# Kernel optimization log

Hardware: AMD Instinct MI355X
Metric: run time of the kernel (lower is better)

## Reference

```python
import jax, jax.numpy as jnp
import numpy as np
from jax import lax

NPOINT = 1024
NSAMPLE = 32
RADIUS = 0.2
EPS = 1e-5  # BatchNorm eps (torch default)
MLP = [64, 64, 128]
IN_CHANNEL = 6  # 3 (relative xyz) + 3 (point features)


def setup_inputs() -> dict:
    key = jax.random.key(0)
    ks = jax.random.split(key, 2 + len(MLP))
    B, N, D = 16, 4096, 3
    inp = {
        "xyz": jax.random.uniform(ks[0], (B, N, 3), jnp.float32),
        "points": jax.random.normal(ks[1], (B, N, D), jnp.float32),
    }
    last = IN_CHANNEL
    for i, co in enumerate(MLP):
        inp[f"w{i}"] = jax.random.normal(ks[2 + i], (co, last), jnp.float32) * (1.0 / np.sqrt(last))
        inp[f"b{i}"] = jnp.zeros((co,), jnp.float32)
        inp[f"gamma{i}"] = jnp.ones((co,), jnp.float32)
        inp[f"beta{i}"] = jnp.zeros((co,), jnp.float32)
        last = co
    return inp


def index_points(points, idx):
    # points: [B, N, C]; idx: [B, S] or [B, S, K] -> [B, S, C] or [B, S, K, C]
    B, C = points.shape[0], points.shape[-1]
    flat = idx.reshape(B, -1)
    out = jnp.take_along_axis(points, flat[:, :, None], axis=1)
    return out.reshape(idx.shape + (C,))


def farthest_point_sample(xyz, npoint):
    # Deterministic FPS (start index 0 per batch); torch version uses a random start.
    B, N, _ = xyz.shape

    def step(carry, _):
        dist, far = carry
        centroid = jnp.take_along_axis(xyz, far[:, None, None], axis=1)  # [B,1,3]
        d = jnp.sum((xyz - centroid) ** 2, axis=-1)  # [B,N]
        dist = jnp.minimum(dist, d)
        return (dist, jnp.argmax(dist, axis=-1).astype(jnp.int32)), far

    init = (jnp.full((B, N), 1e10, dtype=xyz.dtype), jnp.zeros((B,), jnp.int32))
    _, fars = lax.scan(step, init, None, length=npoint)  # [npoint, B]
    return jnp.transpose(fars)  # [B, npoint]


def square_distance(src, dst):
    # [B,N,3] x [B,M,3] -> [B,N,M] squared distances
    d = -2.0 * jnp.einsum('bnc,bmc->bnm', src, dst)
    d = d + jnp.sum(src ** 2, -1)[:, :, None]
    d = d + jnp.sum(dst ** 2, -1)[:, None, :]
    return d


def query_ball_point(radius, nsample, xyz, new_xyz):
    B, N, _ = xyz.shape
    sqr = square_distance(new_xyz, xyz)  # [B,S,N]
    idx = jnp.broadcast_to(jnp.arange(N, dtype=jnp.int32), sqr.shape)
    idx = jnp.where(sqr > radius ** 2, N, idx)
    idx = jnp.sort(idx, axis=-1)[:, :, :nsample]  # [B,S,nsample]
    first = idx[:, :, :1]
    return jnp.where(idx == N, first, idx)


def reference(xyz, points,
              w0, b0, gamma0, beta0,
              w1, b1, gamma1, beta1,
              w2, b2, gamma2, beta2):
    fps_idx = farthest_point_sample(xyz, NPOINT)          # [B,S]
    new_xyz = index_points(xyz, fps_idx)                  # [B,S,3]
    idx = query_ball_point(RADIUS, NSAMPLE, xyz, new_xyz)  # [B,S,K]
    grouped_xyz = index_points(xyz, idx) - new_xyz[:, :, None, :]  # [B,S,K,3]
    grouped_pts = index_points(points, idx)               # [B,S,K,D]
    x = jnp.concatenate([grouped_xyz, grouped_pts], axis=-1)  # [B,S,K,3+D]

    for (w, b, g, be) in [(w0, b0, gamma0, beta0),
                          (w1, b1, gamma1, beta1),
                          (w2, b2, gamma2, beta2)]:
        x = jnp.einsum('bskc,oc->bsko', x, w) + b  # 1x1 Conv2d
        mean = x.mean(axis=(0, 1, 2))
        var = x.var(axis=(0, 1, 2))  # biased, matches BN training-mode normalization
        x = jax.nn.relu(g * (x - mean) * lax.rsqrt(var + EPS) + be)

    new_points = x.max(axis=2)  # max-pool over the K neighbor dim -> [B,S,mlp[-1]]
    return new_xyz, new_points
```

## Files before the change

kernel.cpp:

```cpp
#include <hip/hip_runtime.h>
#include <hip/hip_fp16.h>
#include <stdint.h>

#define B_ 16
#define N_ 4096
#define S_ 1024
#define K_ 32
#define NQ_ (B_*S_)
#define NPIX_ (NQ_*K_)
#define OUTNP_ (NQ_*3)
#define EPS_ 1e-5f


#define DPPMAX64(x, CTRL) do { \
  unsigned _lo = (unsigned)(x); unsigned _hi = (unsigned)((x)>>32); \
  unsigned _plo = (unsigned)__builtin_amdgcn_update_dpp((int)_lo,(int)_lo,(CTRL),0xF,0xF,false); \
  unsigned _phi = (unsigned)__builtin_amdgcn_update_dpp((int)_hi,(int)_hi,(CTRL),0xF,0xF,false); \
  unsigned long long _p = (((unsigned long long)_phi)<<32)|_plo; \
  if (_p > (x)) (x) = _p; \
} while(0)

#define DPPMAXF(r, CTRL) do { \
  float _t = __int_as_float(__builtin_amdgcn_update_dpp(__float_as_int(r),__float_as_int(r),(CTRL),0xF,0xF,false)); \
  (r) = fmaxf((r), _t); \
} while(0)

__global__ __launch_bounds__(512) void k_fps(const float* __restrict__ xyz,
                                             float* __restrict__ out,
                                             float* __restrict__ nx) {
  const int b = blockIdx.x;
  const int t = threadIdx.x;
  const int lane = t & 63, wid = t >> 6;
  __shared__ int SX[N_], SY[N_], SZ[N_];
  __shared__ unsigned long long kbuf[2][8];
  const float* xb = xyz + (size_t)b * N_ * 3;
  for (int j = t; j < N_; j += 512) {
    SX[j] = (int)(xb[j*3+0] * 536870912.0f);
    SY[j] = (int)(xb[j*3+1] * 536870912.0f);
    SZ[j] = (int)(xb[j*3+2] * 536870912.0f);
  }
  __syncthreads();
  int PX[8], PY[8], PZ[8];
  unsigned long long key[8];
#pragma unroll
  for (int i = 0; i < 8; ++i) {
    const int j = t*8 + i;
    PX[i] = SX[j]; PY[i] = SY[j]; PZ[i] = SZ[j];
    key[i] = ~0ull;
  }
  int far = 0, farA = 0, farB = 0;
  for (int it = 0; it < S_; ++it) {
    if (it == t)       farA = far;
    if (it == t + 512) farB = far;
    if (it == S_-1) break;
    const int cx = SX[far], cy = SY[far], cz = SZ[far];
    unsigned long long best = 0;
#pragma unroll
    for (int i = 0; i < 8; ++i) {
      const int dx = PX[i]-cx, dy = PY[i]-cy, dz = PZ[i]-cz;
      unsigned long long nk = (unsigned long long)(unsigned)(4095 - (t*8 + i));
      nk += (unsigned long long)((long long)dx*dx);
      nk += (unsigned long long)((long long)dy*dy);
      nk += (unsigned long long)((long long)dz*dz);
      if (nk < key[i]) key[i] = nk;
      if (key[i] > best) best = key[i];
    }
    DPPMAX64(best, 0x111);
    DPPMAX64(best, 0x112);
    DPPMAX64(best, 0x114);
    DPPMAX64(best, 0x118);
    DPPMAX64(best, 0x142);
    DPPMAX64(best, 0x143);
    if (lane == 63) kbuf[it & 1][wid] = best;
    __syncthreads();
    unsigned long long g = kbuf[it & 1][lane & 7];
    DPPMAX64(g, 0x111); DPPMAX64(g, 0x112); DPPMAX64(g, 0x114);
    far = 4095 - (__builtin_amdgcn_readlane((int)(unsigned)g, 7) & 4095);
  }
  {
    const float s = 1.862645149230957e-9f;
    const float ax = (float)SX[farA]*s, ay = (float)SY[farA]*s, az = (float)SZ[farA]*s;
    const float bx = (float)SX[farB]*s, by = (float)SY[farB]*s, bz = (float)SZ[farB]*s;
    const int oA = (b*S_ + t)*3;
    const int oB = (b*S_ + t + 512)*3;
    out[oA] = ax; out[oA+1] = ay; out[oA+2] = az;
    nx[oA]  = ax; nx[oA+1]  = ay; nx[oA+2]  = az;
    out[oB] = bx; out[oB+1] = by; out[oB+2] = bz;
    nx[oB]  = bx; nx[oB+1]  = by; nx[oB+2]  = bz;
  }
}

__global__ __launch_bounds__(256) void k_ball(const float* __restrict__ xyz,
                                              const float* __restrict__ nx,
                                              int* __restrict__ idx,
                                              const float* __restrict__ w0,
                                              const float* __restrict__ w1,
                                              const float* __restrict__ w2,
                                              float* __restrict__ w0t,
                                              float* __restrict__ w1t,
                                              float* __restrict__ w2t) {
  if (blockIdx.x == NQ_/4) {
    const int t = threadIdx.x;
    for (int i = t; i < 64*6; i += 256)  { int o = i/6,  c = i%6;  w0t[c*64  + o] = w0[i]; }
    for (int i = t; i < 64*64; i += 256) { int o = i>>6, c = i&63; w1t[c*64  + o] = w1[i]; }
    for (int i = t; i < 128*64; i += 256){ int o = i>>6, c = i&63; w2t[c*128 + o] = w2[i]; }
    return;
  }
  const int lane = threadIdx.x & 63;
  const int q = blockIdx.x * 4 + (threadIdx.x >> 6);
  const int b = q >> 10;
  const float* xb = xyz + (size_t)b * N_ * 3;
  const double qx = (double)nx[q*3+0], qy = (double)nx[q*3+1], qz = (double)nx[q*3+2];
  const double qq = qx*qx + qy*qy + qz*qz;
  const double r2 = 0.2 * 0.2;
  int found = 0, first_j = 0;
  bool have_first = false;
  for (int c = 0; c < N_/64; ++c) {
    const int j = c*64 + lane;
    const double px = (double)xb[j*3+0], py = (double)xb[j*3+1], pz = (double)xb[j*3+2];
    const double dot = px*qx + py*qy + pz*qz;
    const double pp  = px*px + py*py + pz*pz;
    const double d   = qq + pp - 2.0*dot;
    const bool hit = (d <= r2);
    const unsigned long long mask = __ballot(hit);
    if (!have_first && mask) { first_j = c*64 + (__ffsll(mask) - 1); have_first = true; }
    const int pos = found + (int)__popcll(mask & ((1ull << lane) - 1ull));
    if (hit && pos < K_) idx[q*K_ + pos] = j;
    found += (int)__popcll(mask);
    if (found >= K_) break;
  }
  const int cnt = found < K_ ? found : K_;
  if (lane >= cnt && lane < K_) idx[q*K_ + lane] = first_j;
}

__global__ __launch_bounds__(256) void k_momw(const float* __restrict__ xyz,
                                              const float* __restrict__ points,
                                              const float* __restrict__ nx,
                                              const int* __restrict__ idx,
                                              float* __restrict__ momp) {
  const int tid = blockIdx.x * blockDim.x + threadIdx.x;
  float m[6] = {0,0,0,0,0,0};
  float M2[21];
#pragma unroll
  for (int u = 0; u < 21; ++u) M2[u] = 0.0f;
  int js[8], qs[8];
#pragma unroll
  for (int r = 0; r < 8; ++r) {
    const int pix = tid + (r << 16);
    js[r] = idx[pix]; qs[r] = pix >> 5;
  }
#pragma unroll
  for (int r = 0; r < 8; ++r) {
    const int b = qs[r] >> 10;
    const float* xp = xyz    + (size_t)(b*N_ + js[r])*3;
    const float* pq = points + (size_t)(b*N_ + js[r])*3;
    const float* nq = nx + qs[r]*3;
    float g[6];
    g[0] = xp[0]-nq[0]; g[1] = xp[1]-nq[1]; g[2] = xp[2]-nq[2];
    g[3] = pq[0]; g[4] = pq[1]; g[5] = pq[2];
#pragma unroll
    for (int i = 0; i < 6; ++i) m[i] += g[i];
    int u = 0;
#pragma unroll
    for (int i = 0; i < 6; ++i)
#pragma unroll
      for (int jj = i; jj < 6; ++jj) { M2[u] = fmaf(g[i], g[jj], M2[u]); ++u; }
  }
#pragma unroll
  for (int i = 0; i < 6; ++i)
#pragma unroll
    for (int s = 1; s < 64; s <<= 1) m[i] += __shfl_xor(m[i], s);
#pragma unroll
  for (int u = 0; u < 21; ++u)
#pragma unroll
    for (int s = 1; s < 64; s <<= 1) M2[u] += __shfl_xor(M2[u], s);
  if ((threadIdx.x & 63) == 0) {
    const int w = blockIdx.x * 4 + (threadIdx.x >> 6);
    float* dst = momp + w*32;
#pragma unroll
    for (int i = 0; i < 6; ++i) dst[i] = m[i];
#pragma unroll
    for (int u = 0; u < 21; ++u) dst[6+u] = M2[u];
  }
}

__global__ void k_fin0r(const float* __restrict__ momp,
                        const float* __restrict__ w0, const float* __restrict__ b0,
                        const float* __restrict__ g0, const float* __restrict__ be0,
                        float* __restrict__ pr) {
  __shared__ float part[8][32];
  __shared__ float red[32];
  const int t = threadIdx.x;
  const int c = t & 31, p = t >> 5;
  float a = 0.f;
  for (int w = p; w < 1024; w += 8) a += momp[w*32 + c];
  part[p][c] = a;
  __syncthreads();
  if (t < 32) {
    float s = 0.f;
#pragma unroll
    for (int pp = 0; pp < 8; ++pp) s += part[pp][c];
    red[c] = s;
  }
  __syncthreads();
  if (t < 64) {
    const float inv = 1.0f / (float)NPIX_;
    float m1[6];
#pragma unroll
    for (int i = 0; i < 6; ++i) m1[i] = red[i] * inv;
    float M2[6][6];
    int u = 0;
#pragma unroll
    for (int i = 0; i < 6; ++i)
#pragma unroll
      for (int jj = i; jj < 6; ++jj) { float v = red[6+u]*inv; M2[i][jj] = v; M2[jj][i] = v; ++u; }
    float w[6];
#pragma unroll
    for (int i = 0; i < 6; ++i) w[i] = w0[t*6+i];
    float ml = 0.0f;
#pragma unroll
    for (int i = 0; i < 6; ++i) ml += w[i]*m1[i];
    float e2 = 0.0f;
#pragma unroll
    for (int i = 0; i < 6; ++i)
#pragma unroll
      for (int jj = 0; jj < 6; ++jj) e2 += w[i]*w[jj]*M2[i][jj];
    const float var = e2 - ml*ml;
    const float mean = ml + b0[t];
    const float sc = g0[t] * rsqrtf(var + EPS_);
    pr[t] = sc; pr[64+t] = be0[t] - mean*sc;
  }
}

__global__ void k_fin1r(const float* __restrict__ s1p,
                        const float* __restrict__ g1, const float* __restrict__ be1,
                        float* __restrict__ pr) {
  __shared__ float pa[4][64], pb[4][64];
  const int t = threadIdx.x;
  const int c = t & 63, p = t >> 6;
  const int wq = c >> 4, u = c & 15;
  float sa = 0.f, sb = 0.f;
  for (int blk = p; blk < 1024; blk += 4) {
    const int w = blk*4 + wq;
    sa += s1p[w*32 + u];
    sb += s1p[w*32 + 16 + u];
  }
  pa[p][c] = sa; pb[p][c] = sb;
  __syncthreads();
  if (t < 64) {
    const float A  = pa[0][t]+pa[1][t]+pa[2][t]+pa[3][t];
    const float Bq = pb[0][t]+pb[1][t]+pb[2][t]+pb[3][t];
    const float inv = 1.0f / (float)NPIX_;
    const float mean = A*inv;
    const float var = Bq*inv - mean*mean;
    const float sc = g1[t] * rsqrtf(var + EPS_);
    pr[128+t] = sc; pr[192+t] = be1[t] - mean*sc;
  }
}

__global__ void k_fin2r(const float* __restrict__ s2p,
                        const float* __restrict__ g2, const float* __restrict__ be2,
                        float* __restrict__ pr) {
  __shared__ float pa[2][128], pb[2][128];
  const int t = threadIdx.x;
  const int c = t & 127, p = t >> 7;
  const int wq = c >> 5, u = c & 31;
  float sa = 0.f, sb = 0.f;
  for (int blk = p; blk < 1024; blk += 2) {
    const int w = blk*4 + wq;
    sa += s2p[w*64 + u];
    sb += s2p[w*64 + 32 + u];
  }
  pa[p][c] = sa; pb[p][c] = sb;
  __syncthreads();
  if (t < 128) {
    const float A  = pa[0][t]+pa[1][t];
    const float Bq = pb[0][t]+pb[1][t];
    const float inv = 1.0f / (float)NPIX_;
    const float mean = A*inv;
    const float var = Bq*inv - mean*mean;
    const float sc = g2[t] * rsqrtf(var + EPS_);
    pr[256+t] = sc; pr[384+t] = be2[t] - mean*sc;
  }
}

__global__ void k_mom(const float* __restrict__ xyz, const float* __restrict__ points,
                      const float* __restrict__ nx, const int* __restrict__ idx,
                      float* __restrict__ st) {
  const int tid = blockIdx.x * blockDim.x + threadIdx.x;
  float m[6] = {0,0,0,0,0,0};
  float M2[21];
#pragma unroll
  for (int u = 0; u < 21; ++u) M2[u] = 0.0f;
  int js[8], qs[8];
#pragma unroll
  for (int r = 0; r < 8; ++r) { const int pix = tid + (r << 16); js[r] = idx[pix]; qs[r] = pix >> 5; }
#pragma unroll
  for (int r = 0; r < 8; ++r) {
    const int b = qs[r] >> 10;
    const float* xp = xyz    + (size_t)(b*N_ + js[r])*3;
    const float* pq = points + (size_t)(b*N_ + js[r])*3;
    const float* nq = nx + qs[r]*3;
    float g[6];
    g[0] = xp[0]-nq[0]; g[1] = xp[1]-nq[1]; g[2] = xp[2]-nq[2];
    g[3] = pq[0]; g[4] = pq[1]; g[5] = pq[2];
#pragma unroll
    for (int i = 0; i < 6; ++i) m[i] += g[i];
    int u = 0;
#pragma unroll
    for (int i = 0; i < 6; ++i)
#pragma unroll
      for (int jj = i; jj < 6; ++jj) { M2[u] = fmaf(g[i], g[jj], M2[u]); ++u; }
  }
#pragma unroll
  for (int i = 0; i < 6; ++i)
#pragma unroll
    for (int s = 1; s < 64; s <<= 1) m[i] += __shfl_xor(m[i], s);
#pragma unroll
  for (int u = 0; u < 21; ++u)
#pragma unroll
    for (int s = 1; s < 64; s <<= 1) M2[u] += __shfl_xor(M2[u], s);
  if ((threadIdx.x & 63) == 0) {
#pragma unroll
    for (int i = 0; i < 6; ++i) atomicAdd(&st[i], m[i]);
#pragma unroll
    for (int u = 0; u < 21; ++u) atomicAdd(&st[6+u], M2[u]);
  }
}

__global__ void k_fin0(const float* __restrict__ w0, const float* __restrict__ b0,
                       const float* __restrict__ g0, const float* __restrict__ be0,
                       const float* __restrict__ st, float* __restrict__ pr) {
  const int c = threadIdx.x;
  const float inv = 1.0f / (float)NPIX_;
  float m1[6];
#pragma unroll
  for (int i = 0; i < 6; ++i) m1[i] = st[i] * inv;
  float M2[6][6];
  int u = 0;
#pragma unroll
  for (int i = 0; i < 6; ++i)
#pragma unroll
    for (int jj = i; jj < 6; ++jj) { float v = st[6+u]*inv; M2[i][jj] = v; M2[jj][i] = v; ++u; }
  float w[6];
#pragma unroll
  for (int i = 0; i < 6; ++i) w[i] = w0[c*6+i];
  float ml = 0.0f;
#pragma unroll
  for (int i = 0; i < 6; ++i) ml += w[i]*m1[i];
  float e2 = 0.0f;
#pragma unroll
  for (int i = 0; i < 6; ++i)
#pragma unroll
    for (int jj = 0; jj < 6; ++jj) e2 += w[i]*w[jj]*M2[i][jj];
  const float var = e2 - ml*ml;
  const float mean = ml + b0[c];
  const float sc = g0[c] * rsqrtf(var + EPS_);
  pr[c] = sc; pr[64+c] = be0[c] - mean*sc;
}

__global__ void k_fin(const float* __restrict__ gam, const float* __restrict__ bet,
                      const float* __restrict__ ssum, const float* __restrict__ ssq,
                      float* __restrict__ psc, float* __restrict__ psh) {
  const int c = threadIdx.x;
  const float inv = 1.0f / (float)NPIX_;
  const float mean = ssum[c]*inv;
  const float var = ssq[c]*inv - mean*mean;
  const float sc = gam[c] * rsqrtf(var + EPS_);
  psc[c] = sc; psh[c] = bet[c] - mean*sc;
}

__global__ __launch_bounds__(256) void k_s1(
    const float* __restrict__ xyz, const float* __restrict__ points,
    const float* __restrict__ nx, const int* __restrict__ idx,
    const float* __restrict__ w0t, const float* __restrict__ w1t,
    const float* __restrict__ b0, const float* __restrict__ b1,
    const float* __restrict__ pr, float* __restrict__ s1p,
    __half* __restrict__ a1)
{
  __shared__ float a0T[64][64];
  const int tid = threadIdx.x;
  const int lane = tid & 63;
  const int wid = __builtin_amdgcn_readfirstlane(tid >> 6);
  const int c0 = wid * 16;
  float b0r[16], b1r[16], p0s[16], p0h[16];
#pragma unroll
  for (int u = 0; u < 16; ++u) {
    b0r[u] = b0[c0+u]; b1r[u] = b1[c0+u];
    p0s[u] = pr[c0+u]; p0h[u] = pr[64+c0+u];
  }
  float s1a[16], s1b[16];
#pragma unroll
  for (int u = 0; u < 16; ++u) { s1a[u] = 0.0f; s1b[u] = 0.0f; }

  for (int tile = blockIdx.x; tile < NQ_/2; tile += gridDim.x) {
    const int q = tile*2 + (lane >> 5);
    const int k = lane & 31;
    const int b = q >> 10;
    const int j = idx[q*K_ + k];
    const float* xp = xyz    + (size_t)(b*N_ + j)*3;
    const float* pp = points + (size_t)(b*N_ + j)*3;
    const float* nq = nx + q*3;
    float g[6];
    g[0] = xp[0]-nq[0]; g[1] = xp[1]-nq[1]; g[2] = xp[2]-nq[2];
    g[3] = pp[0];       g[4] = pp[1];       g[5] = pp[2];
    float acc[16];
#pragma unroll
    for (int u = 0; u < 16; ++u) acc[u] = b0r[u];
#pragma unroll
    for (int i = 0; i < 6; ++i) {
      const float* w = w0t + i*64 + c0;
#pragma unroll
      for (int u = 0; u < 16; ++u) acc[u] = fmaf(w[u], g[i], acc[u]);
    }
#pragma unroll
    for (int u = 0; u < 16; ++u)
      a0T[c0+u][lane] = fmaxf(fmaf(p0s[u], acc[u], p0h[u]), 0.0f);
    __syncthreads();
#pragma unroll
    for (int u = 0; u < 16; ++u) acc[u] = b1r[u];
#pragma unroll 8
    for (int ci = 0; ci < 64; ++ci) {
      const float av = a0T[ci][lane];
      const float* w = w1t + ci*64 + c0;
#pragma unroll
      for (int u = 0; u < 16; ++u) acc[u] = fmaf(w[u], av, acc[u]);
    }
    const int pix = tile*64 + lane;
#pragma unroll
    for (int u = 0; u < 16; ++u) {
      s1a[u] += acc[u]; s1b[u] = fmaf(acc[u], acc[u], s1b[u]);
      a1[(size_t)(c0+u)*NPIX_ + pix] = __float2half(acc[u]);
    }
    __syncthreads();
  }
#pragma unroll
  for (int u = 0; u < 16; ++u) {
    float a = s1a[u], bq = s1b[u];
#pragma unroll
    for (int s = 1; s < 64; s <<= 1) { a += __shfl_xor(a, s); bq += __shfl_xor(bq, s); }
    s1a[u] = a; s1b[u] = bq;
  }
  if (lane == 0) {
    float* dst = s1p + (blockIdx.x*4 + wid)*32;
#pragma unroll
    for (int u = 0; u < 16; ++u) { dst[u] = s1a[u]; dst[16+u] = s1b[u]; }
  }
}

__global__ __launch_bounds__(256) void k_s2(
    const __half* __restrict__ a1, const float* __restrict__ w2t,
    const float* __restrict__ b2, const float* __restrict__ g2,
    const float* __restrict__ pr, float* __restrict__ s2p,
    float* __restrict__ pooled)
{
  __shared__ float a1T[64][64];
  const int tid = threadIdx.x;
  const int lane = tid & 63;
  const int wid = __builtin_amdgcn_readfirstlane(tid >> 6);
  const int cl = wid * 16;
  const int c20 = wid * 32;
  float p1s[16], p1h[16], b2r[32];
  bool g2p[32];
#pragma unroll
  for (int u = 0; u < 16; ++u) { p1s[u] = pr[128+cl+u]; p1h[u] = pr[192+cl+u]; }
#pragma unroll
  for (int u = 0; u < 32; ++u) { b2r[u] = b2[c20+u]; g2p[u] = (g2[c20+u] >= 0.0f); }
  float s2a[32], s2b[32];
#pragma unroll
  for (int u = 0; u < 32; ++u) { s2a[u] = 0.0f; s2b[u] = 0.0f; }

  for (int tile = blockIdx.x; tile < NQ_/2; tile += gridDim.x) {
    const int pixb = tile*64;
#pragma unroll
    for (int u = 0; u < 16; ++u) {
      const float v = __half2float(a1[(size_t)(cl+u)*NPIX_ + pixb + lane]);
      a1T[cl+u][lane] = fmaxf(fmaf(p1s[u], v, p1h[u]), 0.0f);
    }
    __syncthreads();
    float acc2[32];
#pragma unroll
    for (int u = 0; u < 32; ++u) acc2[u] = b2r[u];
#pragma unroll 8
    for (int ci = 0; ci < 64; ++ci) {
      const float av = a1T[ci][lane];
      const float* w = w2t + ci*128 + c20;
#pragma unroll
      for (int u = 0; u < 32; ++u) acc2[u] = fmaf(w[u], av, acc2[u]);
    }
    const int q = tile*2 + (lane >> 5);
#pragma unroll
    for (int u = 0; u < 32; ++u) {
      s2a[u] += acc2[u]; s2b[u] = fmaf(acc2[u], acc2[u], s2b[u]);
      float r = g2p[u] ? acc2[u] : -acc2[u];
      DPPMAXF(r, 0xB1);
      DPPMAXF(r, 0x4E);
      DPPMAXF(r, 0x141);
      DPPMAXF(r, 0x140);
      DPPMAXF(r, 0x142);
      if ((lane & 31) == 31) pooled[q*128 + c20 + u] = g2p[u] ? r : -r;
    }
    __syncthreads();
  }
#pragma unroll
  for (int u = 0; u < 32; ++u) {
    float a = s2a[u], bq = s2b[u];
#pragma unroll
    for (int s = 1; s < 64; s <<= 1) { a += __shfl_xor(a, s); bq += __shfl_xor(bq, s); }
    s2a[u] = a; s2b[u] = bq;
  }
  if (lane == 0) {
    float* dst = s2p + (blockIdx.x*4 + wid)*64;
#pragma unroll
    for (int u = 0; u < 32; ++u) { dst[u] = s2a[u]; dst[32+u] = s2b[u]; }
  }
}

__global__ __launch_bounds__(256) void k_s3(const float* __restrict__ pr,
                                            float* __restrict__ outnp) {
  const int g = blockIdx.x * 256 + threadIdx.x;
  const int c = g & 127;
  const float y = fmaf(pr[256+c], outnp[g], pr[384+c]);
  outnp[g] = fmaxf(y, 0.0f);
}

template<int STAGE>
__global__ __launch_bounds__(256) void k_stage(
    const float* __restrict__ xyz, const float* __restrict__ points,
    const float* __restrict__ nx, const int* __restrict__ idx,
    const float* __restrict__ w0t, const float* __restrict__ w1t,
    const float* __restrict__ w2t,
    const float* __restrict__ b0, const float* __restrict__ b1,
    const float* __restrict__ b2,
    const float* __restrict__ pr, float* __restrict__ st,
    float* __restrict__ out)
{
  __shared__ float gT[6][64];
  __shared__ float a0T[64][64];
  __shared__ float a1T[64][64];
  const int tid = threadIdx.x;
  const int lane = tid & 63;
  const int wid = __builtin_amdgcn_readfirstlane(tid >> 6);
  const int c0 = wid * 16;
  const int c20 = wid * 32;

  float s1a[16], s1b[16], s2a[32], s2b[32];
  if (STAGE == 1) {
#pragma unroll
    for (int u = 0; u < 16; ++u) { s1a[u] = 0.0f; s1b[u] = 0.0f; }
  }
  if (STAGE == 2) {
#pragma unroll
    for (int u = 0; u < 32; ++u) { s2a[u] = 0.0f; s2b[u] = 0.0f; }
  }

  for (int tile = blockIdx.x; tile < NQ_/2; tile += gridDim.x) {
    const int q = tile*2 + (lane >> 5);
    const int k = lane & 31;
    if (wid == 0) {
      const int b = q >> 10;
      const int j = idx[q*K_ + k];
      const float* xp = xyz    + (size_t)(b*N_ + j)*3;
      const float* pp = points + (size_t)(b*N_ + j)*3;
      const float* nq = nx + q*3;
      gT[0][lane] = xp[0]-nq[0]; gT[1][lane] = xp[1]-nq[1]; gT[2][lane] = xp[2]-nq[2];
      gT[3][lane] = pp[0];       gT[4][lane] = pp[1];       gT[5][lane] = pp[2];
    }
    __syncthreads();
    float acc[16];
#pragma unroll
    for (int u = 0; u < 16; ++u) acc[u] = b0[c0+u];
#pragma unroll
    for (int i = 0; i < 6; ++i) {
      const float av = gT[i][lane];
      const float* w = w0t + i*64 + c0;
#pragma unroll
      for (int u = 0; u < 16; ++u) acc[u] = fmaf(w[u], av, acc[u]);
    }
#pragma unroll
    for (int u = 0; u < 16; ++u) {
      const float a = fmaf(pr[c0+u], acc[u], pr[64+c0+u]);
      a0T[c0+u][lane] = fmaxf(a, 0.0f);
    }
    __syncthreads();
#pragma unroll
    for (int u = 0; u < 16; ++u) acc[u] = b1[c0+u];
#pragma unroll 8
    for (int ci = 0; ci < 64; ++ci) {
      const float av = a0T[ci][lane];
      const float* w = w1t + ci*64 + c0;
#pragma unroll
      for (int u = 0; u < 16; ++u) acc[u] = fmaf(w[u], av, acc[u]);
    }
    if (STAGE == 1) {
#pragma unroll
      for (int u = 0; u < 16; ++u) { s1a[u] += acc[u]; s1b[u] = fmaf(acc[u], acc[u], s1b[u]); }
    } else {
#pragma unroll
      for (int u = 0; u < 16; ++u) {
        const float a = fmaf(pr[128+c0+u], acc[u], pr[192+c0+u]);
        a1T[c0+u][lane] = fmaxf(a, 0.0f);
      }
      __syncthreads();
      float acc2[32];
#pragma unroll
      for (int u = 0; u < 32; ++u) acc2[u] = b2[c20+u];
#pragma unroll 8
      for (int ci = 0; ci < 64; ++ci) {
        const float av = a1T[ci][lane];
        const float* w = w2t + ci*128 + c20;
#pragma unroll
        for (int u = 0; u < 32; ++u) acc2[u] = fmaf(w[u], av, acc2[u]);
      }
      if (STAGE == 2) {
#pragma unroll
        for (int u = 0; u < 32; ++u) { s2a[u] += acc2[u]; s2b[u] = fmaf(acc2[u], acc2[u], s2b[u]); }
      } else {
#pragma unroll
        for (int u = 0; u < 32; ++u) {
          float y = fmaf(pr[256+c20+u], acc2[u], pr[384+c20+u]);
#pragma unroll
          for (int s = 1; s < 32; s <<= 1) y = fmaxf(y, __shfl_xor(y, s));
          if ((lane & 31) == 0) out[OUTNP_ + q*128 + c20 + u] = fmaxf(y, 0.0f);
        }
      }
    }
    __syncthreads();
  }
  if (STAGE == 1) {
#pragma unroll
    for (int u = 0; u < 16; ++u) {
      float a = s1a[u], bq = s1b[u];
#pragma unroll
      for (int s = 1; s < 64; s <<= 1) { a += __shfl_xor(a, s); bq += __shfl_xor(bq, s); }
      if (lane == 0) { atomicAdd(&st[32 + c0+u], a); atomicAdd(&st[96 + c0+u], bq); }
    }
  }
  if (STAGE == 2) {
#pragma unroll
    for (int u = 0; u < 32; ++u) {
      float a = s2a[u], bq = s2b[u];
#pragma unroll
      for (int s = 1; s < 64; s <<= 1) { a += __shfl_xor(a, s); bq += __shfl_xor(bq, s); }
      if (lane == 0) { atomicAdd(&st[160 + c20+u], a); atomicAdd(&st[288 + c20+u], bq); }
    }
  }
}

extern "C" void kernel_launch(void* const* d_in, const int* in_sizes, int n_in,
                              void* d_out, int out_size, void* d_ws, size_t ws_size,
                              hipStream_t stream) {
  const float* xyz    = (const float*)d_in[0];
  const float* points = (const float*)d_in[1];
  const float* w0  = (const float*)d_in[2];
  const float* b0  = (const float*)d_in[3];
  const float* g0  = (const float*)d_in[4];
  const float* be0 = (const float*)d_in[5];
  const float* w1  = (const float*)d_in[6];
  const float* b1  = (const float*)d_in[7];
  const float* g1  = (const float*)d_in[8];
  const float* be1 = (const float*)d_in[9];
  const float* w2  = (const float*)d_in[10];
  const float* b2  = (const float*)d_in[11];
  const float* g2  = (const float*)d_in[12];
  const float* be2 = (const float*)d_in[13];
  float* out = (float*)d_out;
  float* ws  = (float*)d_ws;

  float* nx  = ws;
  int*   idx = (int*)(ws + 49152);
  float* w0t = ws + 573440;
  float* w1t = ws + 573824;
  float* w2t = ws + 577920;
  float* st  = ws + 586112;
  float* pr  = ws + 586624;
  __half* a1 = (__half*)(ws + 2684928);
  float* momp = ws + 587264;
  float* s1p  = ws + 587264 + 32768;
  float* s2p  = (float*)(ws + 49152);
  float* pooled = out + OUTNP_;

  const size_t need = (size_t)(2684928) * sizeof(float) + (size_t)33554432 * sizeof(__half);
  const bool big = ws_size >= need;

  k_fps<<<B_, 512, 0, stream>>>(xyz, out, nx);
  k_ball<<<NQ_/4 + 1, 256, 0, stream>>>(xyz, nx, idx, w0, w1, w2, w0t, w1t, w2t);
  if (big) {
    k_momw<<<256, 256, 0, stream>>>(xyz, points, nx, idx, momp);
    k_fin0r<<<1, 256, 0, stream>>>(momp, w0, b0, g0, be0, pr);
    k_s1<<<1024, 256, 0, stream>>>(xyz, points, nx, idx, w0t, w1t, b0, b1, pr, s1p, a1);
    k_fin1r<<<1, 256, 0, stream>>>(s1p, g1, be1, pr);
    k_s2<<<1024, 256, 0, stream>>>(a1, w2t, b2, g2, pr, s2p, pooled);
    k_fin2r<<<1, 256, 0, stream>>>(s2p, g2, be2, pr);
    k_s3<<<NPIX_*4/256, 256, 0, stream>>>(pr, pooled);
  } else {
    hipMemsetAsync(st, 0, 512*sizeof(float), stream);
    k_mom<<<256, 256, 0, stream>>>(xyz, points, nx, idx, st);
    k_fin0<<<1, 64, 0, stream>>>(w0, b0, g0, be0, st, pr);
    k_stage<1><<<1024, 256, 0, stream>>>(xyz, points, nx, idx, w0t, w1t, w2t, b0, b1, b2, pr, st, out);
    k_fin<<<1, 64, 0, stream>>>(g1, be1, st+32, st+96, pr+128, pr+192);
    k_stage<2><<<1024, 256, 0, stream>>>(xyz, points, nx, idx, w0t, w1t, w2t, b0, b1, b2, pr, st, out);
    k_fin<<<1, 128, 0, stream>>>(g2, be2, st+160, st+288, pr+256, pr+384);
    k_stage<3><<<1024, 256, 0, stream>>>(xyz, points, nx, idx, w0t, w1t, w2t, b0, b1, b2, pr, st, out);
  }
}
```

Measured before the change: 1.249 ms.

## Fuse post-FPS pipeline into a single cooperative persistent kernel with grid syncs

Merges ball query, moment statistics, the BN finalizations and the two MLP stages plus the final scale into one cooperative kernel separated by grid-wide syncs. This removes several kernel launches and their inter-kernel gaps, and sizes the grid from occupancy. Finalization steps run on block 0 while other blocks wait at the barrier. The small-workspace fallback path is removed, and a multi-kernel path is kept if the cooperative launch fails.

```diff
diff --git a/kernel.cpp b/kernel.cpp
--- a/kernel.cpp
+++ b/kernel.cpp
@@ -1,6 +1,9 @@
 #include <hip/hip_runtime.h>
 #include <hip/hip_fp16.h>
+#include <hip/hip_cooperative_groups.h>
 #include <stdint.h>
+
+namespace cg = cooperative_groups;
 
 #define B_ 16
 #define N_ 4096
@@ -10,7 +13,6 @@
 #define NPIX_ (NQ_*K_)
 #define OUTNP_ (NQ_*3)
 #define EPS_ 1e-5f
-
 
 #define DPPMAX64(x, CTRL) do { \
   unsigned _lo = (unsigned)(x); unsigned _hi = (unsigned)((x)>>32); \
@@ -90,24 +92,10 @@
   }
 }
 
-__global__ __launch_bounds__(256) void k_ball(const float* __restrict__ xyz,
-                                              const float* __restrict__ nx,
-                                              int* __restrict__ idx,
-                                              const float* __restrict__ w0,
-                                              const float* __restrict__ w1,
-                                              const float* __restrict__ w2,
-                                              float* __restrict__ w0t,
-                                              float* __restrict__ w1t,
-                                              float* __restrict__ w2t) {
-  if (blockIdx.x == NQ_/4) {
-    const int t = threadIdx.x;
-    for (int i = t; i < 64*6; i += 256)  { int o = i/6,  c = i%6;  w0t[c*64  + o] = w0[i]; }
-    for (int i = t; i < 64*64; i += 256) { int o = i>>6, c = i&63; w1t[c*64  + o] = w1[i]; }
-    for (int i = t; i < 128*64; i += 256){ int o = i>>6, c = i&63; w2t[c*128 + o] = w2[i]; }
-    return;
-  }
-  const int lane = threadIdx.x & 63;
-  const int q = blockIdx.x * 4 + (threadIdx.x >> 6);
+__device__ inline void ball_one(const int q, const int lane,
+                                const float* __restrict__ xyz,
+                                const float* __restrict__ nx,
+                                int* __restrict__ idx) {
   const int b = q >> 10;
   const float* xb = xyz + (size_t)b * N_ * 3;
   const double qx = (double)nx[q*3+0], qy = (double)nx[q*3+1], qz = (double)nx[q*3+2];
@@ -133,6 +121,324 @@
   if (lane >= cnt && lane < K_) idx[q*K_ + lane] = first_j;
 }
 
+__global__ __launch_bounds__(256) void k_mega(
+    const float* __restrict__ xyz, const float* __restrict__ points,
+    const float* __restrict__ w0, const float* __restrict__ b0,
+    const float* __restrict__ g0, const float* __restrict__ be0,
+    const float* __restrict__ w1, const float* __restrict__ b1,
+    const float* __restrict__ g1, const float* __restrict__ be1,
+    const float* __restrict__ w2, const float* __restrict__ b2,
+    const float* __restrict__ g2, const float* __restrict__ be2,
+    float* __restrict__ nx, int* __restrict__ idx,
+    float* __restrict__ w0t, float* __restrict__ w1t, float* __restrict__ w2t,
+    float* __restrict__ pr, float* __restrict__ momp,
+    float* __restrict__ s1p, float* __restrict__ s2p,
+    __half* __restrict__ a1, float* __restrict__ pooled)
+{
+  cg::grid_group gridg = cg::this_grid();
+  __shared__ float smem[64][64];
+  float* sm = &smem[0][0];
+  const int tid = threadIdx.x;
+  const int lane = tid & 63;
+  const int wid = __builtin_amdgcn_readfirstlane(tid >> 6);
+  const int nb = gridDim.x, bid = blockIdx.x;
+  const int nwave = nb * 4, wgid = bid*4 + wid;
+
+  if (bid == 0) {
+    for (int i = tid; i < 64*6; i += 256)  { int o = i/6,  c = i%6;  w0t[c*64  + o] = w0[i]; }
+    for (int i = tid; i < 64*64; i += 256) { int o = i>>6, c = i&63; w1t[c*64  + o] = w1[i]; }
+    for (int i = tid; i < 128*64; i += 256){ int o = i>>6, c = i&63; w2t[c*128 + o] = w2[i]; }
+  }
+  for (int q = wgid; q < NQ_; q += nwave) ball_one(q, lane, xyz, nx, idx);
+  gridg.sync();
+
+  {
+    float m[6] = {0,0,0,0,0,0};
+    float M2[21];
+#pragma unroll
+    for (int u = 0; u < 21; ++u) M2[u] = 0.0f;
+    for (int pix = bid*256 + tid; pix < NPIX_; pix += nb*256) {
+      const int q = pix >> 5;
+      const int b = q >> 10;
+      const int j = idx[pix];
+      const float* xp = xyz    + (size_t)(b*N_ + j)*3;
+      const float* pq = points + (size_t)(b*N_ + j)*3;
+      const float* nq = nx + q*3;
+      float g[6];
+      g[0] = xp[0]-nq[0]; g[1] = xp[1]-nq[1]; g[2] = xp[2]-nq[2];
+      g[3] = pq[0]; g[4] = pq[1]; g[5] = pq[2];
+#pragma unroll
+      for (int i = 0; i < 6; ++i) m[i] += g[i];
+      int u = 0;
+#pragma unroll
+      for (int i = 0; i < 6; ++i)
+#pragma unroll
+        for (int jj = i; jj < 6; ++jj) { M2[u] = fmaf(g[i], g[jj], M2[u]); ++u; }
+    }
+#pragma unroll
+    for (int i = 0; i < 6; ++i)
+#pragma unroll
+      for (int s = 1; s < 64; s <<= 1) m[i] += __shfl_xor(m[i], s);
+#pragma unroll
+    for (int u = 0; u < 21; ++u)
+#pragma unroll
+      for (int s = 1; s < 64; s <<= 1) M2[u] += __shfl_xor(M2[u], s);
+    if (lane == 0) {
+      float* dst = sm + wid*32;
+#pragma unroll
+      for (int i = 0; i < 6; ++i) dst[i] = m[i];
+#pragma unroll
+      for (int u = 0; u < 21; ++u) dst[6+u] = M2[u];
+#pragma unroll
+      for (int u = 27; u < 32; ++u) dst[u] = 0.0f;
+    }
+    __syncthreads();
+    if (tid < 32) momp[bid*32 + tid] = sm[tid] + sm[32+tid] + sm[64+tid] + sm[96+tid];
+  }
+  gridg.sync();
+
+  if (bid == 0) {
+    const int c = tid & 31, p = tid >> 5;
+    float a = 0.f;
+    for (int w = p; w < nb; w += 8) a += momp[w*32 + c];
+    sm[p*32 + c] = a;
+    __syncthreads();
+    if (tid < 32) {
+      float s = 0.f;
+#pragma unroll
+      for (int pp = 0; pp < 8; ++pp) s += sm[pp*32 + c];
+      sm[256 + c] = s;
+    }
+    __syncthreads();
+    if (tid < 64) {
+      const float inv = 1.0f / (float)NPIX_;
+      float m1[6];
+#pragma unroll
+      for (int i = 0; i < 6; ++i) m1[i] = sm[256+i] * inv;
+      float M2[6][6];
+      int u = 0;
+#pragma unroll
+      for (int i = 0; i < 6; ++i)
+#pragma unroll
+        for (int jj = i; jj < 6; ++jj) { float v = sm[256+6+u]*inv; M2[i][jj] = v; M2[jj][i] = v; ++u; }
+      float w[6];
+#pragma unroll
+      for (int i = 0; i < 6; ++i) w[i] = w0[tid*6+i];
+      float ml = 0.0f;
+#pragma unroll
+      for (int i = 0; i < 6; ++i) ml += w[i]*m1[i];
+      float e2 = 0.0f;
+#pragma unroll
+      for (int i = 0; i < 6; ++i)
+#pragma unroll
+        for (int jj = 0; jj < 6; ++jj) e2 += w[i]*w[jj]*M2[i][jj];
+      const float var = e2 - ml*ml;
+      const float mean = ml + b0[tid];
+      const float sc = g0[tid] * rsqrtf(var + EPS_);
+      pr[tid] = sc; pr[64+tid] = be0[tid] - mean*sc;
+    }
+  }
+  gridg.sync();
+
+  {
+    const int c0 = wid * 16;
+    float b0r[16], b1r[16], p0s[16], p0h[16];
+#pragma unroll
+    for (int u = 0; u < 16; ++u) {
+      b0r[u] = b0[c0+u]; b1r[u] = b1[c0+u];
+      p0s[u] = pr[c0+u]; p0h[u] = pr[64+c0+u];
+    }
+    float s1a[16], s1b[16];
+#pragma unroll
+    for (int u = 0; u < 16; ++u) { s1a[u] = 0.0f; s1b[u] = 0.0f; }
+    for (int tile = bid; tile < NQ_/2; tile += nb) {
+      const int q = tile*2 + (lane >> 5);
+      const int k = lane & 31;
+      const int b = q >> 10;
+      const int j = idx[q*K_ + k];
+      const float* xp = xyz    + (size_t)(b*N_ + j)*3;
+      const float* pp = points + (size_t)(b*N_ + j)*3;
+      const float* nq = nx + q*3;
+      float g[6];
+      g[0] = xp[0]-nq[0]; g[1] = xp[1]-nq[1]; g[2] = xp[2]-nq[2];
+      g[3] = pp[0];       g[4] = pp[1];       g[5] = pp[2];
+      float acc[16];
+#pragma unroll
+      for (int u = 0; u < 16; ++u) acc[u] = b0r[u];
+#pragma unroll
+      for (int i = 0; i < 6; ++i) {
+        const float* w = w0t + i*64 + c0;
+#pragma unroll
+        for (int u = 0; u < 16; ++u) acc[u] = fmaf(w[u], g[i], acc[u]);
+      }
+#pragma unroll
+      for (int u = 0; u < 16; ++u)
+        smem[c0+u][lane] = fmaxf(fmaf(p0s[u], acc[u], p0h[u]), 0.0f);
+      __syncthreads();
+#pragma unroll
+      for (int u = 0; u < 16; ++u) acc[u] = b1r[u];
+#pragma unroll 8
+      for (int ci = 0; ci < 64; ++ci) {
+        const float av = smem[ci][lane];
+        const float* w = w1t + ci*64 + c0;
+#pragma unroll
+        for (int u = 0; u < 16; ++u) acc[u] = fmaf(w[u], av, acc[u]);
+      }
+      const int pix = tile*64 + lane;
+#pragma unroll
+      for (int u = 0; u < 16; ++u) {
+        s1a[u] += acc[u]; s1b[u] = fmaf(acc[u], acc[u], s1b[u]);
+        a1[(size_t)(c0+u)*NPIX_ + pix] = __float2half(acc[u]);
+      }
+      __syncthreads();
+    }
+#pragma unroll
+    for (int u = 0; u < 16; ++u) {
+      float a = s1a[u], bq = s1b[u];
+#pragma unroll
+      for (int s = 1; s < 64; s <<= 1) { a += __shfl_xor(a, s); bq += __shfl_xor(bq, s); }
+      s1a[u] = a; s1b[u] = bq;
+    }
+    if (lane == 0) {
+      float* dst = s1p + (bid*4 + wid)*32;
+#pragma unroll
+      for (int u = 0; u < 16; ++u) { dst[u] = s1a[u]; dst[16+u] = s1b[u]; }
+    }
+  }
+  gridg.sync();
+
+  if (bid == 0) {
+    const int c = tid & 63, p = tid >> 6;
+    const int wq = c >> 4, u = c & 15;
+    float sa = 0.f, sb = 0.f;
+    for (int blk = p; blk < nb; blk += 4) {
+      const int w = blk*4 + wq;
+      sa += s1p[w*32 + u];
+      sb += s1p[w*32 + 16 + u];
+    }
+    sm[p*64 + c] = sa; sm[256 + p*64 + c] = sb;
+    __syncthreads();
+    if (tid < 64) {
+      const float A  = sm[tid] + sm[64+tid] + sm[128+tid] + sm[192+tid];
+      const float Bq = sm[256+tid] + sm[256+64+tid] + sm[256+128+tid] + sm[256+192+tid];
+      const float inv = 1.0f / (float)NPIX_;
+      const float mean = A*inv;
+      const float var = Bq*inv - mean*mean;
+      const float sc = g1[tid] * rsqrtf(var + EPS_);
+      pr[128+tid] = sc; pr[192+tid] = be1[tid] - mean*sc;
+    }
+  }
+  gridg.sync();
+
+  {
+    const int cl = wid * 16;
+    const int c20 = wid * 32;
+    float p1s[16], p1h[16], b2r[32];
+    bool g2p[32];
+#pragma unroll
+    for (int u = 0; u < 16; ++u) { p1s[u] = pr[128+cl+u]; p1h[u] = pr[192+cl+u]; }
+#pragma unroll
+    for (int u = 0; u < 32; ++u) { b2r[u] = b2[c20+u]; g2p[u] = (g2[c20+u] >= 0.0f); }
+    float s2a[32], s2b[32];
+#pragma unroll
+    for (int u = 0; u < 32; ++u) { s2a[u] = 0.0f; s2b[u] = 0.0f; }
+    for (int tile = bid; tile < NQ_/2; tile += nb) {
+      const int pixb = tile*64;
+#pragma unroll
+      for (int u = 0; u < 16; ++u) {
+        const float v = __half2float(a1[(size_t)(cl+u)*NPIX_ + pixb + lane]);
+        smem[cl+u][lane] = fmaxf(fmaf(p1s[u], v, p1h[u]), 0.0f);
+      }
+      __syncthreads();
+      float acc2[32];
+#pragma unroll
+      for (int u = 0; u < 32; ++u) acc2[u] = b2r[u];
+#pragma unroll 8
+      for (int ci = 0; ci < 64; ++ci) {
+        const float av = smem[ci][lane];
+        const float* w = w2t + ci*128 + c20;
+#pragma unroll
+        for (int u = 0; u < 32; ++u) acc2[u] = fmaf(w[u], av, acc2[u]);
+      }
+      const int q = tile*2 + (lane >> 5);
+#pragma unroll
+      for (int u = 0; u < 32; ++u) {
+        s2a[u] += acc2[u]; s2b[u] = fmaf(acc2[u], acc2[u], s2b[u]);
+        float r = g2p[u] ? acc2[u] : -acc2[u];
+        DPPMAXF(r, 0xB1);
+        DPPMAXF(r, 0x4E);
+        DPPMAXF(r, 0x141);
+        DPPMAXF(r, 0x140);
+        DPPMAXF(r, 0x142);
+        if ((lane & 31) == 31) pooled[q*128 + c20 + u] = g2p[u] ? r : -r;
+      }
+      __syncthreads();
+    }
+#pragma unroll
+    for (int u = 0; u < 32; ++u) {
+      float a = s2a[u], bq = s2b[u];
+#pragma unroll
+      for (int s = 1; s < 64; s <<= 1) { a += __shfl_xor(a, s); bq += __shfl_xor(bq, s); }
+      s2a[u] = a; s2b[u] = bq;
+    }
+    if (lane == 0) {
+      float* dst = s2p + (bid*4 + wid)*64;
+#pragma unroll
+      for (int u = 0; u < 32; ++u) { dst[u] = s2a[u]; dst[32+u] = s2b[u]; }
+    }
+  }
+  gridg.sync();
+
+  if (bid == 0) {
+    const int c = tid & 127, p = tid >> 7;
+    const int wq = c >> 5, u = c & 31;
+    float sa = 0.f, sb = 0.f;
+    for (int blk = p; blk < nb; blk += 2) {
+      const int w = blk*4 + wq;
+      sa += s2p[w*64 + u];
+      sb += s2p[w*64 + 32 + u];
+    }
+    sm[p*128 + c] = sa; sm[256 + p*128 + c] = sb;
+    __syncthreads();
+    if (tid < 128) {
+      const float A  = sm[tid] + sm[128+tid];
+      const float Bq = sm[256+tid] + sm[256+128+tid];
+      const float inv = 1.0f / (float)NPIX_;
+      const float mean = A*inv;
+      const float var = Bq*inv - mean*mean;
+      const float sc = g2[tid] * rsqrtf(var + EPS_);
+      pr[256+tid] = sc; pr[384+tid] = be2[tid] - mean*sc;
+    }
+  }
+  gridg.sync();
+
+  for (int g = bid*256 + tid; g < NQ_*128; g += nb*256) {
+    const int c = g & 127;
+    pooled[g] = fmaxf(fmaf(pr[256+c], pooled[g], pr[384+c]), 0.0f);
+  }
+}
+
+__global__ __launch_bounds__(256) void k_ball(const float* __restrict__ xyz,
+                                              const float* __restrict__ nx,
+                                              int* __restrict__ idx,
+                                              const float* __restrict__ w0,
+                                              const float* __restrict__ w1,
+                                              const float* __restrict__ w2,
+                                              float* __restrict__ w0t,
+                                              float* __restrict__ w1t,
+                                              float* __restrict__ w2t) {
+  if (blockIdx.x == NQ_/4) {
+    const int t = threadIdx.x;
+    for (int i = t; i < 64*6; i += 256)  { int o = i/6,  c = i%6;  w0t[c*64  + o] = w0[i]; }
+    for (int i = t; i < 64*64; i += 256) { int o = i>>6, c = i&63; w1t[c*64  + o] = w1[i]; }
+    for (int i = t; i < 128*64; i += 256){ int o = i>>6, c = i&63; w2t[c*128 + o] = w2[i]; }
+    return;
+  }
+  const int lane = threadIdx.x & 63;
+  const int q = blockIdx.x * 4 + (threadIdx.x >> 6);
+  ball_one(q, lane, xyz, nx, idx);
+}
+
 __global__ __launch_bounds__(256) void k_momw(const float* __restrict__ xyz,
                                               const float* __restrict__ points,
                                               const float* __restrict__ nx,
@@ -187,13 +493,13 @@
 __global__ void k_fin0r(const float* __restrict__ momp,
                         const float* __restrict__ w0, const float* __restrict__ b0,
                         const float* __restrict__ g0, const float* __restrict__ be0,
-                        float* __restrict__ pr) {
+                        float* __restrict__ pr, int nent) {
   __shared__ float part[8][32];
   __shared__ float red[32];
   const int t = threadIdx.x;
   const int c = t & 31, p = t >> 5;
   float a = 0.f;
-  for (int w = p; w < 1024; w += 8) a += momp[w*32 + c];
+  for (int w = p; w < nent; w += 8) a += momp[w*32 + c];
   part[p][c] = a;
   __syncthreads();
   if (t < 32) {
@@ -234,13 +540,13 @@
 
 __global__ void k_fin1r(const float* __restrict__ s1p,
                         const float* __restrict__ g1, const float* __restrict__ be1,
-                        float* __restrict__ pr) {
+                        float* __restrict__ pr, int nblk) {
   __shared__ float pa[4][64], pb[4][64];
   const int t = threadIdx.x;
   const int c = t & 63, p = t >> 6;
   const int wq = c >> 4, u = c & 15;
   float sa = 0.f, sb = 0.f;
-  for (int blk = p; blk < 1024; blk += 4) {
+  for (int blk = p; blk < nblk; blk += 4) {
     const int w = blk*4 + wq;
     sa += s1p[w*32 + u];
     sb += s1p[w*32 + 16 + u];
@@ -260,13 +566,13 @@
 
 __global__ void k_fin2r(const float* __restrict__ s2p,
                         const float* __restrict__ g2, const float* __restrict__ be2,
-                        float* __restrict__ pr) {
+                        float* __restrict__ pr, int nblk) {
   __shared__ float pa[2][128], pb[2][128];
   const int t = threadIdx.x;
   const int c = t & 127, p = t >> 7;
   const int wq = c >> 5, u = c & 31;
   float sa = 0.f, sb = 0.f;
-  for (int blk = p; blk < 1024; blk += 2) {
+  for (int blk = p; blk < nblk; blk += 2) {
     const int w = blk*4 + wq;
     sa += s2p[w*64 + u];
     sb += s2p[w*64 + 32 + u];
@@ -282,92 +588,6 @@
     const float sc = g2[t] * rsqrtf(var + EPS_);
     pr[256+t] = sc; pr[384+t] = be2[t] - mean*sc;
   }
-}
-
-__global__ void k_mom(const float* __restrict__ xyz, const float* __restrict__ points,
-                      const float* __restrict__ nx, const int* __restrict__ idx,
-                      float* __restrict__ st) {
-  const int tid = blockIdx.x * blockDim.x + threadIdx.x;
-  float m[6] = {0,0,0,0,0,0};
-  float M2[21];
-#pragma unroll
-  for (int u = 0; u < 21; ++u) M2[u] = 0.0f;
-  int js[8], qs[8];
-#pragma unroll
-  for (int r = 0; r < 8; ++r) { const int pix = tid + (r << 16); js[r] = idx[pix]; qs[r] = pix >> 5; }
-#pragma unroll
-  for (int r = 0; r < 8; ++r) {
-    const int b = qs[r] >> 10;
-    const float* xp = xyz    + (size_t)(b*N_ + js[r])*3;
-    const float* pq = points + (size_t)(b*N_ + js[r])*3;
-    const float* nq = nx + qs[r]*3;
-    float g[6];
-    g[0] = xp[0]-nq[0]; g[1] = xp[1]-nq[1]; g[2] = xp[2]-nq[2];
-    g[3] = pq[0]; g[4] = pq[1]; g[5] = pq[2];
-#pragma unroll
-    for (int i = 0; i < 6; ++i) m[i] += g[i];
-    int u = 0;
-#pragma unroll
-    for (int i = 0; i < 6; ++i)
-#pragma unroll
-      for (int jj = i; jj < 6; ++jj) { M2[u] = fmaf(g[i], g[jj], M2[u]); ++u; }
-  }
-#pragma unroll
-  for (int i = 0; i < 6; ++i)
-#pragma unroll
-    for (int s = 1; s < 64; s <<= 1) m[i] += __shfl_xor(m[i], s);
-#pragma unroll
-  for (int u = 0; u < 21; ++u)
-#pragma unroll
-    for (int s = 1; s < 64; s <<= 1) M2[u] += __shfl_xor(M2[u], s);
-  if ((threadIdx.x & 63) == 0) {
-#pragma unroll
-    for (int i = 0; i < 6; ++i) atomicAdd(&st[i], m[i]);
-#pragma unroll
-    for (int u = 0; u < 21; ++u) atomicAdd(&st[6+u], M2[u]);
-  }
-}
-
-__global__ void k_fin0(const float* __restrict__ w0, const float* __restrict__ b0,
-                       const float* __restrict__ g0, const float* __restrict__ be0,
-                       const float* __restrict__ st, float* __restrict__ pr) {
-  const int c = threadIdx.x;
-  const float inv = 1.0f / (float)NPIX_;
-  float m1[6];
-#pragma unroll
-  for (int i = 0; i < 6; ++i) m1[i] = st[i] * inv;
-  float M2[6][6];
-  int u = 0;
-#pragma unroll
-  for (int i = 0; i < 6; ++i)
-#pragma unroll
-    for (int jj = i; jj < 6; ++jj) { float v = st[6+u]*inv; M2[i][jj] = v; M2[jj][i] = v; ++u; }
-  float w[6];
-#pragma unroll
-  for (int i = 0; i < 6; ++i) w[i] = w0[c*6+i];
-  float ml = 0.0f;
-#pragma unroll
-  for (int i = 0; i < 6; ++i) ml += w[i]*m1[i];
-  float e2 = 0.0f;
-#pragma unroll
-  for (int i = 0; i < 6; ++i)
-#pragma unroll
-    for (int jj = 0; jj < 6; ++jj) e2 += w[i]*w[jj]*M2[i][jj];
-  const float var = e2 - ml*ml;
-  const float mean = ml + b0[c];
-  const float sc = g0[c] * rsqrtf(var + EPS_);
-  pr[c] = sc; pr[64+c] = be0[c] - mean*sc;
-}
-
-__global__ void k_fin(const float* __restrict__ gam, const float* __restrict__ bet,
-                      const float* __restrict__ ssum, const float* __restrict__ ssq,
-                      float* __restrict__ psc, float* __restrict__ psh) {
-  const int c = threadIdx.x;
-  const float inv = 1.0f / (float)NPIX_;
-  const float mean = ssum[c]*inv;
-  const float var = ssq[c]*inv - mean*mean;
-  const float sc = gam[c] * rsqrtf(var + EPS_);
-  psc[c] = sc; psh[c] = bet[c] - mean*sc;
 }
 
 __global__ __launch_bounds__(256) void k_s1(
@@ -392,7 +612,6 @@
   float s1a[16], s1b[16];
 #pragma unroll
   for (int u = 0; u < 16; ++u) { s1a[u] = 0.0f; s1b[u] = 0.0f; }
-
   for (int tile = blockIdx.x; tile < NQ_/2; tile += gridDim.x) {
     const int q = tile*2 + (lane >> 5);
     const int k = lane & 31;
@@ -469,7 +688,6 @@
   float s2a[32], s2b[32];
 #pragma unroll
   for (int u = 0; u < 32; ++u) { s2a[u] = 0.0f; s2b[u] = 0.0f; }
-
   for (int tile = blockIdx.x; tile < NQ_/2; tile += gridDim.x) {
     const int pixb = tile*64;
 #pragma unroll
@@ -522,129 +740,6 @@
   const int c = g & 127;
   const float y = fmaf(pr[256+c], outnp[g], pr[384+c]);
   outnp[g] = fmaxf(y, 0.0f);
-}
-
-template<int STAGE>
-__global__ __launch_bounds__(256) void k_stage(
-    const float* __restrict__ xyz, const float* __restrict__ points,
-    const float* __restrict__ nx, const int* __restrict__ idx,
-    const float* __restrict__ w0t, const float* __restrict__ w1t,
-    const float* __restrict__ w2t,
-    const float* __restrict__ b0, const float* __restrict__ b1,
-    const float* __restrict__ b2,
-    const float* __restrict__ pr, float* __restrict__ st,
-    float* __restrict__ out)
-{
-  __shared__ float gT[6][64];
-  __shared__ float a0T[64][64];
-  __shared__ float a1T[64][64];
-  const int tid = threadIdx.x;
-  const int lane = tid & 63;
-  const int wid = __builtin_amdgcn_readfirstlane(tid >> 6);
-  const int c0 = wid * 16;
-  const int c20 = wid * 32;
-
-  float s1a[16], s1b[16], s2a[32], s2b[32];
-  if (STAGE == 1) {
-#pragma unroll
-    for (int u = 0; u < 16; ++u) { s1a[u] = 0.0f; s1b[u] = 0.0f; }
-  }
-  if (STAGE == 2) {
-#pragma unroll
-    for (int u = 0; u < 32; ++u) { s2a[u] = 0.0f; s2b[u] = 0.0f; }
-  }
-
-  for (int tile = blockIdx.x; tile < NQ_/2; tile += gridDim.x) {
-    const int q = tile*2 + (lane >> 5);
-    const int k = lane & 31;
-    if (wid == 0) {
-      const int b = q >> 10;
-      const int j = idx[q*K_ + k];
-      const float* xp = xyz    + (size_t)(b*N_ + j)*3;
-      const float* pp = points + (size_t)(b*N_ + j)*3;
-      const float* nq = nx + q*3;
-      gT[0][lane] = xp[0]-nq[0]; gT[1][lane] = xp[1]-nq[1]; gT[2][lane] = xp[2]-nq[2];
-      gT[3][lane] = pp[0];       gT[4][lane] = pp[1];       gT[5][lane] = pp[2];
-    }
-    __syncthreads();
-    float acc[16];
-#pragma unroll
-    for (int u = 0; u < 16; ++u) acc[u] = b0[c0+u];
-#pragma unroll
-    for (int i = 0; i < 6; ++i) {
-      const float av = gT[i][lane];
-      const float* w = w0t + i*64 + c0;
-#pragma unroll
-      for (int u = 0; u < 16; ++u) acc[u] = fmaf(w[u], av, acc[u]);
-    }
-#pragma unroll
-    for (int u = 0; u < 16; ++u) {
-      const float a = fmaf(pr[c0+u], acc[u], pr[64+c0+u]);
-      a0T[c0+u][lane] = fmaxf(a, 0.0f);
-    }
-    __syncthreads();
-#pragma unroll
-    for (int u = 0; u < 16; ++u) acc[u] = b1[c0+u];
-#pragma unroll 8
-    for (int ci = 0; ci < 64; ++ci) {
-      const float av = a0T[ci][lane];
-      const float* w = w1t + ci*64 + c0;
-#pragma unroll
-      for (int u = 0; u < 16; ++u) acc[u] = fmaf(w[u], av, acc[u]);
-    }
-    if (STAGE == 1) {
-#pragma unroll
-      for (int u = 0; u < 16; ++u) { s1a[u] += acc[u]; s1b[u] = fmaf(acc[u], acc[u], s1b[u]); }
-    } else {
-#pragma unroll
-      for (int u = 0; u < 16; ++u) {
-        const float a = fmaf(pr[128+c0+u], acc[u], pr[192+c0+u]);
-        a1T[c0+u][lane] = fmaxf(a, 0.0f);
-      }
-      __syncthreads();
-      float acc2[32];
-#pragma unroll
-      for (int u = 0; u < 32; ++u) acc2[u] = b2[c20+u];
-#pragma unroll 8
-      for (int ci = 0; ci < 64; ++ci) {
-        const float av = a1T[ci][lane];
-        const float* w = w2t + ci*128 + c20;
-#pragma unroll
-        for (int u = 0; u < 32; ++u) acc2[u] = fmaf(w[u], av, acc2[u]);
-      }
-      if (STAGE == 2) {
-#pragma unroll
-        for (int u = 0; u < 32; ++u) { s2a[u] += acc2[u]; s2b[u] = fmaf(acc2[u], acc2[u], s2b[u]); }
-      } else {
-#pragma unroll
-        for (int u = 0; u < 32; ++u) {
-          float y = fmaf(pr[256+c20+u], acc2[u], pr[384+c20+u]);
-#pragma unroll
-          for (int s = 1; s < 32; s <<= 1) y = fmaxf(y, __shfl_xor(y, s));
-          if ((lane & 31) == 0) out[OUTNP_ + q*128 + c20 + u] = fmaxf(y, 0.0f);
-        }
-      }
-    }
-    __syncthreads();
-  }
-  if (STAGE == 1) {
-#pragma unroll
-    for (int u = 0; u < 16; ++u) {
-      float a = s1a[u], bq = s1b[u];
-#pragma unroll
-      for (int s = 1; s < 64; s <<= 1) { a += __shfl_xor(a, s); bq += __shfl_xor(bq, s); }
-      if (lane == 0) { atomicAdd(&st[32 + c0+u], a); atomicAdd(&st[96 + c0+u], bq); }
-    }
-  }
-  if (STAGE == 2) {
-#pragma unroll
-    for (int u = 0; u < 32; ++u) {
-      float a = s2a[u], bq = s2b[u];
-#pragma unroll
-      for (int s = 1; s < 64; s <<= 1) { a += __shfl_xor(a, s); bq += __shfl_xor(bq, s); }
-      if (lane == 0) { atomicAdd(&st[160 + c20+u], a); atomicAdd(&st[288 + c20+u], bq); }
-    }
-  }
 }
 
 extern "C" void kernel_launch(void* const* d_in, const int* in_sizes, int n_in,
@@ -672,7 +767,6 @@
   float* w0t = ws + 573440;
   float* w1t = ws + 573824;
   float* w2t = ws + 577920;
-  float* st  = ws + 586112;
   float* pr  = ws + 586624;
   __half* a1 = (__half*)(ws + 2684928);
   float* momp = ws + 587264;
@@ -684,23 +778,38 @@
   const bool big = ws_size >= need;
 
   k_fps<<<B_, 512, 0, stream>>>(xyz, out, nx);
-  k_ball<<<NQ_/4 + 1, 256, 0, stream>>>(xyz, nx, idx, w0, w1, w2, w0t, w1t, w2t);
+
+  bool done = false;
   if (big) {
+    int occ = 0;
+    if (hipOccupancyMaxActiveBlocksPerMultiprocessor(&occ, k_mega, 256, 0) == hipSuccess && occ > 0) {
+      int nb = occ * 256;
+      if (nb > 1024) nb = 1024;
+      void* args[] = {
+        (void*)&xyz, (void*)&points,
+        (void*)&w0, (void*)&b0, (void*)&g0, (void*)&be0,
+        (void*)&w1, (void*)&b1, (void*)&g1, (void*)&be1,
+        (void*)&w2, (void*)&b2, (void*)&g2, (void*)&be2,
+        (void*)&nx, (void*)&idx,
+        (void*)&w0t, (void*)&w1t, (void*)&w2t,
+        (void*)&pr, (void*)&momp, (void*)&s1p, (void*)&s2p,
+        (void*)&a1, (void*)&pooled
+      };
+      if (hipLaunchCooperativeKernel((const void*)k_mega, dim3(nb), dim3(256),
+                                     args, 0, stream) == hipSuccess) {
+        done = true;
+      }
+    }
+  }
+  if (!done && big) {
+    const int NB = 1024;
+    k_ball<<<NQ_/4 + 1, 256, 0, stream>>>(xyz, nx, idx, w0, w1, w2, w0t, w1t, w2t);
     k_momw<<<256, 256, 0, stream>>>(xyz, points, nx, idx, momp);
-    k_fin0r<<<1, 256, 0, stream>>>(momp, w0, b0, g0, be0, pr);
-    k_s1<<<1024, 256, 0, stream>>>(xyz, points, nx, idx, w0t, w1t, b0, b1, pr, s1p, a1);
-    k_fin1r<<<1, 256, 0, stream>>>(s1p, g1, be1, pr);
-    k_s2<<<1024, 256, 0, stream>>>(a1, w2t, b2, g2, pr, s2p, pooled);
-    k_fin2r<<<1, 256, 0, stream>>>(s2p, g2, be2, pr);
+    k_fin0r<<<1, 256, 0, stream>>>(momp, w0, b0, g0, be0, pr, 1024);
+    k_s1<<<NB, 256, 0, stream>>>(xyz, points, nx, idx, w0t, w1t, b0, b1, pr, s1p, a1);
+    k_fin1r<<<1, 256, 0, stream>>>(s1p, g1, be1, pr, NB);
+    k_s2<<<NB, 256, 0, stream>>>(a1, w2t, b2, g2, pr, s2p, pooled);
+    k_fin2r<<<1, 256, 0, stream>>>(s2p, g2, be2, pr, NB);
     k_s3<<<NPIX_*4/256, 256, 0, stream>>>(pr, pooled);
-  } else {
-    hipMemsetAsync(st, 0, 512*sizeof(float), stream);
-    k_mom<<<256, 256, 0, stream>>>(xyz, points, nx, idx, st);
-    k_fin0<<<1, 64, 0, stream>>>(w0, b0, g0, be0, st, pr);
-    k_stage<1><<<1024, 256, 0, stream>>>(xyz, points, nx, idx, w0t, w1t, w2t, b0, b1, b2, pr, st, out);
-    k_fin<<<1, 64, 0, stream>>>(g1, be1, st+32, st+96, pr+128, pr+192);
-    k_stage<2><<<1024, 256, 0, stream>>>(xyz, points, nx, idx, w0t, w1t, w2t, b0, b1, b2, pr, st, out);
-    k_fin<<<1, 128, 0, stream>>>(g2, be2, st+160, st+288, pr+256, pr+384);
-    k_stage<3><<<1024, 256, 0, stream>>>(xyz, points, nx, idx, w0t, w1t, w2t, b0, b1, b2, pr, st, out);
-  }
-}
+  }
+}
```

Result: slower. 2.098 ms (+67.9%).
